# Performance work log

Hardware: AMD Instinct MI355X
Metric: run time of the kernel (lower is better)

Reference implementation:

```python
import jax, jax.numpy as jnp
import numpy as np

KX, KY = 3, 3
NUM_T_BINS, NUM_F_BINS = 1024, 1024
NX, NY = 512, 512
BATCH, CH = 16, 4


def fitpack_knots(x, k):
    # left/right: (k+1) repeated boundary knots; interior: sliding mean of x[i+1:i+k+1]
    n = x.shape[0]
    cs = jnp.concatenate([jnp.zeros((1,), x.dtype), jnp.cumsum(x)])
    interior = (cs[k + 1:n] - cs[1:n - k]) / k  # length n-k-1
    left = jnp.full((k + 1,), x[0], x.dtype)
    right = jnp.full((k + 1,), x[-1], x.dtype)
    return jnp.concatenate([left, interior, right])  # length n+k+1


def bspline_basis(x, k, t):
    # Cox-de Boor recursion; returns [n_points, m] with m = len(t)-k-1
    n = x.shape[0]
    m = t.shape[0] - k - 1
    b = ((t[None, :m] <= x[:, None]) & (x[:, None] < t[None, 1:m + 1])).astype(x.dtype)
    b = b.at[:, 0].set(jnp.where(x < t[1], 1.0, b[:, 0]))
    b = b.at[:, m - 1].set(jnp.where(x >= t[-2], 1.0, b[:, m - 1]))
    for d in range(1, k + 1):
        ld = t[d:m + d] - t[:m]
        rd = t[d + 1:m + d + 1] - t[1:m + 1]
        L = jnp.where(ld[None, :] == 0, 0.0,
                      (x[:, None] - t[None, :m]) / jnp.where(ld == 0, 1.0, ld)[None, :])
        R = jnp.where(rd[None, :] == 0, 0.0,
                      (t[None, d + 1:m + d + 1] - x[:, None]) / jnp.where(rd == 0, 1.0, rd)[None, :])
        b_shift = jnp.concatenate([b[:, 1:], jnp.zeros((n, 1), x.dtype)], axis=1)
        b = L * b + R * b_shift
    return b


def setup_inputs() -> dict:
    key = jax.random.key(0)
    Z = jax.random.normal(key, (BATCH, CH, NX, NY), dtype=jnp.float32)
    return {"Z": Z}


def reference(Z):
    B, C, nx, ny = Z.shape
    dt = Z.dtype
    # input grids (xin/yin/freqs None, logf False -> linspace(-1,1))
    x = jnp.linspace(-1.0, 1.0, nx, dtype=dt)
    y = jnp.linspace(-1.0, 1.0, ny, dtype=dt)
    tx = fitpack_knots(x, KX)
    ty = fitpack_knots(y, KY)
    Bx = bspline_basis(x, KX, tx)   # [nx, mx] with mx = nx
    By = bspline_basis(y, KY, ty)   # [ny, my] with my = ny
    # fit: least squares via normal equations (sx = sy = 0 -> no ridge term)
    BxT_Z_By = jnp.einsum('ij,bcik,kl->bcjl', Bx, Z, By)          # [B,C,mx,my]
    E = jnp.linalg.solve(Bx.T @ Bx, BxT_Z_By)                      # [B,C,mx,my]
    Coef = jnp.swapaxes(jnp.linalg.solve(By.T @ By, jnp.swapaxes(E, -1, -2)), -1, -2)
    # evaluation grids (xout/yout None, logf False -> linspace(-1,1)), clamped to knot range
    xe = jnp.clip(jnp.linspace(-1.0, 1.0, NUM_T_BINS, dtype=dt), tx[0], tx[-1])
    ye = jnp.clip(jnp.linspace(-1.0, 1.0, NUM_F_BINS, dtype=dt), ty[0], ty[-1])
    Bxe = bspline_basis(xe, KX, tx)  # [num_t, mx]
    Bye = bspline_basis(ye, KY, ty)  # [num_f, my]
    Zi = jnp.einsum('xk,bckm,ym->bcxy', Bxe, Coef, Bye)           # [B,C,num_t,num_f]
    return jnp.transpose(Zi, (0, 1, 3, 2))                         # [B,C,num_f,num_t]
```

## Files before the change

### kernel.cpp

```cpp
#include <hip/hip_runtime.h>

#define NN  512
#define NE  1024
#define NBC 64
#define WH  8
#define WT  17
#define YT  16

typedef float v4f __attribute__((ext_vector_type(4)));


struct Tables {
  float Gb[NN][WT];
  int   espan[NE];
  float ebas[NE * 4];
  float W3[NE][12];
};

constexpr int cfindspan(double u, const float* t) {
  if (u >= (double)t[NN]) return NN - 1;
  int lo = 3, hi = NN - 1;
  while (lo < hi) {
    int mid = (lo + hi + 1) >> 1;
    if ((double)t[mid] <= u) lo = mid; else hi = mid - 1;
  }
  return lo;
}

constexpr void cdeboor4(double u, const float* t, int s, double* N) {
  double left[4] = {}, right[4] = {};
  N[0] = 1.0; N[1] = 0.0; N[2] = 0.0; N[3] = 0.0;
  for (int d = 1; d <= 3; ++d) {
    left[d]  = u - (double)t[s + 1 - d];
    right[d] = (double)t[s + d] - u;
    double saved = 0.0;
    for (int r = 0; r < d; ++r) {
      double temp = N[r] / (right[r + 1] + left[d - r]);
      N[r] = saved + right[r + 1] * temp;
      saved = left[d - r] * temp;
    }
    N[d] = saved;
  }
}

constexpr Tables make_tables() {
  Tables T{};
  float x[NN] = {};
  for (int i = 0; i < NN; ++i) x[i] = (float)(-1.0 + (2.0 * i) / 511.0);
  x[0] = -1.0f; x[NN - 1] = 1.0f;
  float t[NN + 4] = {};
  {
    float cs[NN + 1] = {};
    for (int i = 0; i < NN; ++i) cs[i + 1] = cs[i] + x[i];
    for (int i = 0; i < NN - 4; ++i) t[4 + i] = (cs[4 + i] - cs[1 + i]) / 3.0f;
    for (int i = 0; i < 4; ++i) { t[i] = -1.0f; t[NN + i] = 1.0f; }
  }
  double W[NN][7] = {};
  for (int r = 0; r < NN; ++r) {
    double u = (double)x[r];
    int s = cfindspan(u, t);
    double N[4] = {};
    cdeboor4(u, t, s, N);
    for (int dd = 0; dd < 4; ++dd) W[r][s - r + dd] += N[dd];
  }
  for (int r = 0; r < NN; ++r) {
    double rd = 1.0 / W[r][3];
    for (int k = 1; k <= 3; ++k) {
      if (r + k < NN) {
        double l = W[r + k][3 - k] * rd;
        W[r + k][3 - k] = l;
        for (int cc = 1; cc <= 3; ++cc) W[r + k][3 - k + cc] -= l * W[r][3 + cc];
      }
    }
  }
  double Gbd[NN][WT] = {};
  double tv[WT] = {};
  for (int pass = 0; pass < 3; ++pass) {
    const int ylo = (pass == 0) ? 0 : (pass == 1) ? 480 : 256;
    const int yhi = (pass == 0) ? 32 : (pass == 1) ? 512 : 257;
    for (int y = ylo; y < yhi; ++y) {
      double wv[21] = {};
      int rend = y + 20; if (rend > NN - 1) rend = NN - 1;
      wv[0] = 1.0;
      for (int r = y + 1; r <= rend; ++r) {
        double acc = 0.0;
        if (r - 1 >= y) acc += W[r][2] * wv[r - 1 - y];
        if (r - 2 >= y) acc += W[r][1] * wv[r - 2 - y];
        if (r - 3 >= y) acc += W[r][0] * wv[r - 3 - y];
        wv[r - y] = -acc;
      }
      double g[29] = {};
      int glo = y - WH; if (glo < 0) glo = 0;
      for (int r = rend; r >= glo; --r) {
        double acc = (r >= y) ? wv[r - y] : 0.0;
        if (r + 1 <= rend) acc -= W[r][4] * g[r + 1 - (y - WH)];
        if (r + 2 <= rend) acc -= W[r][5] * g[r + 2 - (y - WH)];
        if (r + 3 <= rend) acc -= W[r][6] * g[r + 3 - (y - WH)];
        g[r - (y - WH)] = acc / W[r][3];
      }
      if (pass == 2) {
        for (int d = 0; d < WT; ++d) tv[d] = g[16 - d];
      } else {
        int jlo = y - WH; if (jlo < 0) jlo = 0;
        int jhi = y + WH; if (jhi > NN - 1) jhi = NN - 1;
        for (int j = jlo; j <= jhi; ++j) {
          const bool bdry = (pass == 0) ? (j < 24) : (j >= 488);
          if (bdry) Gbd[j][y - j + WH] = g[j - (y - WH)];
        }
      }
    }
  }
  for (int j = 24; j < 488; ++j)
    for (int d = 0; d < WT; ++d) Gbd[j][d] = tv[d];
  for (int j = 0; j < NN; ++j)
    for (int d = 0; d < WT; ++d) T.Gb[j][d] = (float)Gbd[j][d];
  int    s_all[NE] = {};
  double dN[NE][4] = {};
  for (int i = 0; i < NE; ++i) {
    float xe = (float)(-1.0 + (2.0 * i) / 1023.0);
    if (i == 0) xe = -1.0f;
    if (i == NE - 1) xe = 1.0f;
    double u = (double)xe;
    int s = cfindspan(u, t);
    double N[4] = {};
    cdeboor4(u, t, s, N);
    s_all[i] = s;
    for (int k = 0; k < 4; ++k) dN[i][k] = N[k];
    T.espan[i] = s;
    T.ebas[i * 4 + 0] = (float)N[0];
    T.ebas[i * 4 + 1] = (float)N[1];
    T.ebas[i * 4 + 2] = (float)N[2];
    T.ebas[i * 4 + 3] = (float)N[3];
  }
  for (int xx = 0; xx < NE; ++xx) {
    const int a3 = (s_all[(xx >> 2) << 2] - 3) & ~3;
    for (int k = 0; k < 4; ++k) {
      const int m = s_all[xx] - 3 + k - a3;
      T.W3[xx][m] = (float)dN[xx][k];
    }
  }
  return T;
}

__constant__ Tables g_tab = make_tables();


__global__ __launch_bounds__(256) void k_solve2d(const float* __restrict__ Z,
                                                 float* __restrict__ CT) {
  const int it = blockIdx.x * 64;
  const int jt = blockIdx.y * 64;
  const int bc = blockIdx.z;
  const float* __restrict__ src = Z + (size_t)bc * (NN * NN);
  __shared__ float At[64][89];
  const int tid = threadIdx.x;
  const int q4 = (tid & 15) * 4;

  {
    float cy[4][WT];
    #pragma unroll
    for (int q = 0; q < 4; ++q)
      #pragma unroll
      for (int d = 0; d < WT; ++d)
        cy[q][d] = g_tab.Gb[jt + q4 + q][d];
    #pragma unroll 1
    for (int p = 0; p < 5; ++p) {
      const int ii = p * 16 + (tid >> 4);
      int gi = it - 8 + ii;
      gi = (gi < 0) ? 0 : ((gi > NN - 1) ? NN - 1 : gi);
      const float* __restrict__ rowp = &src[(size_t)gi * NN];
      float w[20];
      #pragma unroll
      for (int e = 0; e < 5; ++e) {
        int gj = jt + q4 - 8 + e * 4;
        gj = (gj < 0) ? 0 : ((gj > NN - 4) ? NN - 4 : gj);
        *(float4*)&w[e * 4] = *(const float4*)&rowp[gj];
      }
      float4 a = make_float4(0.f, 0.f, 0.f, 0.f);
      #pragma unroll
      for (int d = 0; d < WT; ++d) {
        a.x += cy[0][d] * w[0 + d];
        a.y += cy[1][d] * w[1 + d];
        a.z += cy[2][d] * w[2 + d];
        a.w += cy[3][d] * w[3 + d];
      }
      At[q4 + 0][ii] = a.x;
      At[q4 + 1][ii] = a.y;
      At[q4 + 2][ii] = a.z;
      At[q4 + 3][ii] = a.w;
    }
  }
  {
    float cx[4][WT];
    #pragma unroll
    for (int q = 0; q < 4; ++q)
      #pragma unroll
      for (int d = 0; d < WT; ++d)
        cx[q][d] = g_tab.Gb[it + q4 + q][d];
    __syncthreads();
    float* __restrict__ dst = CT + (size_t)bc * (NN * NN);
    #pragma unroll 1
    for (int p = 0; p < 4; ++p) {
      const int jc = p * 16 + (tid >> 4);
      float w[20];
      #pragma unroll
      for (int e = 0; e < 5; ++e)
        *(float4*)&w[e * 4] = *(const float4*)&At[jc][q4 + e * 4];
      float4 a = make_float4(0.f, 0.f, 0.f, 0.f);
      #pragma unroll
      for (int d = 0; d < WT; ++d) {
        a.x += cx[0][d] * w[0 + d];
        a.y += cx[1][d] * w[1 + d];
        a.z += cx[2][d] * w[2 + d];
        a.w += cx[3][d] * w[3 + d];
      }
      *(float4*)&dst[(size_t)(jt + jc) * NN + it + q4] = a;
    }
  }
}


__global__ __launch_bounds__(256) void k_eval7(const float* __restrict__ CT,
                                               float* __restrict__ out) {
  const int ytile = ((blockIdx.x & 7) << 3) | (blockIdx.x >> 3);
  const int y0 = ytile * YT;
  const int bc = blockIdx.y;
  const float* __restrict__ S = CT + (size_t)bc * (NN * NN);
  __shared__ float rows[14][524];
  const int tid = threadIdx.x;
  const int rlo = g_tab.espan[y0] - 3;

  for (int u = tid; u < 14 * 128; u += 256) {
    const int rr = u >> 7, c4 = (u & 127) * 4;
    const int r = rlo + rr;
    float4 v = (r < NN) ? *(const float4*)&S[(size_t)r * NN + c4]
                        : make_float4(0.f, 0.f, 0.f, 0.f);
    *(float4*)&rows[rr][c4] = v;
  }
  if (tid < 42) {
    const int rr = tid / 3, c4 = 512 + (tid % 3) * 4;
    *(float4*)&rows[rr][c4] = make_float4(0.f, 0.f, 0.f, 0.f);
  }

  const int x0 = tid * 4;
  const int a3 = (g_tab.espan[x0] - 3) & ~3;
  float tp[4][12];
  #pragma unroll
  for (int e = 0; e < 4; ++e)
    #pragma unroll
    for (int m = 0; m < 12; ++m)
      tp[e][m] = g_tab.W3[x0 + e][m];

  __syncthreads();

  auto filterP = [&](int r) -> v4f {
    float w[12];
    #pragma unroll
    for (int e = 0; e < 3; ++e)
      *(float4*)&w[e * 4] = *(const float4*)&rows[r][a3 + e * 4];
    v4f p;
    #pragma unroll
    for (int e = 0; e < 4; ++e) {
      float s0 = 0.f, s1 = 0.f;
      #pragma unroll
      for (int m = 0; m < 12; m += 2) {
        s0 += tp[e][m]     * w[m];
        s1 += tp[e][m + 1] * w[m + 1];
      }
      p[e] = s0 + s1;
    }
    return p;
  };

  v4f P0 = filterP(0), P1 = filterP(1), P2 = filterP(2), P3 = filterP(3);
  int prev = 3;
  float* __restrict__ O0 = out + ((size_t)bc * NE + y0) * NE + x0;
  #pragma unroll 1
  for (int k = 0; k < YT; ++k) {
    const int ry = g_tab.espan[y0 + k] - rlo;
    if (ry != prev) {
      P0 = P1; P1 = P2; P2 = P3;
      P3 = filterP(ry);
      prev = ry;
    }
    const float4 wy = *(const float4*)&g_tab.ebas[(y0 + k) * 4];
    v4f o;
    #pragma unroll
    for (int e = 0; e < 4; ++e)
      o[e] = wy.x * P0[e] + wy.y * P1[e] + wy.z * P2[e] + wy.w * P3[e];
    __builtin_nontemporal_store(o, (v4f*)&O0[(size_t)k * NE]);
  }
}


extern "C" void kernel_launch(void* const* d_in, const int* in_sizes, int n_in,
                              void* d_out, int out_size, void* d_ws, size_t ws_size,
                              hipStream_t stream) {
  (void)in_sizes; (void)n_in; (void)out_size; (void)ws_size;
  const float* Z = (const float*)d_in[0];
  float* out = (float*)d_out;
  float* CT = (float*)d_ws;

  k_solve2d<<<dim3(8, 8, NBC),    256, 0, stream>>>(Z,  CT);
  k_eval7  <<<dim3(NE / YT, NBC), 256, 0, stream>>>(CT, out);
}
```

Baseline: 115.2 us.

## Store intermediate spline coefficients as bf16 and enlarge eval row tile

The solve kernel now writes the coefficient workspace as bfloat16 instead of float32, which halves its write traffic and the eval kernel's read traffic. The eval kernel unpacks bf16 from shared memory with shifts and masks, and each block covers 32 output rows instead of 16, with a matching staged-row count and block swizzle. Fewer blocks reload overlapping coefficient rows. The cost is reduced precision in the intermediate coefficients, which may break accuracy tolerance, and fewer, larger eval blocks.

Measured after the change: 113.1 us. Within noise of the previous version (-1.8%).

```diff
diff --git a/kernel.cpp b/kernel.cpp
--- a/kernel.cpp
+++ b/kernel.cpp
@@ -1,11 +1,13 @@
 #include <hip/hip_runtime.h>
+#include <hip/hip_bf16.h>
 
 #define NN  512
 #define NE  1024
 #define NBC 64
 #define WH  8
 #define WT  17
-#define YT  16
+#define YT  32
+#define NR  20
 
 typedef float v4f __attribute__((ext_vector_type(4)));
 
@@ -144,9 +146,14 @@
 
 __constant__ Tables g_tab = make_tables();
 
+__device__ __forceinline__ unsigned short f2bf(float f) {
+  __hip_bfloat16 h = __float2bfloat16(f);
+  return reinterpret_cast<const unsigned short&>(h);
+}
+
 
 __global__ __launch_bounds__(256) void k_solve2d(const float* __restrict__ Z,
-                                                 float* __restrict__ CT) {
+                                                 unsigned short* __restrict__ CT) {
   const int it = blockIdx.x * 64;
   const int jt = blockIdx.y * 64;
   const int bc = blockIdx.z;
@@ -197,7 +204,7 @@
       for (int d = 0; d < WT; ++d)
         cx[q][d] = g_tab.Gb[it + q4 + q][d];
     __syncthreads();
-    float* __restrict__ dst = CT + (size_t)bc * (NN * NN);
+    unsigned short* __restrict__ dst = CT + (size_t)bc * (NN * NN);
     #pragma unroll 1
     for (int p = 0; p < 4; ++p) {
       const int jc = p * 16 + (tid >> 4);
@@ -213,32 +220,31 @@
         a.z += cx[2][d] * w[2 + d];
         a.w += cx[3][d] * w[3 + d];
       }
-      *(float4*)&dst[(size_t)(jt + jc) * NN + it + q4] = a;
-    }
-  }
-}
-
-
-__global__ __launch_bounds__(256) void k_eval7(const float* __restrict__ CT,
+      ushort4 o;
+      o.x = f2bf(a.x); o.y = f2bf(a.y); o.z = f2bf(a.z); o.w = f2bf(a.w);
+      *(ushort4*)&dst[(size_t)(jt + jc) * NN + it + q4] = o;
+    }
+  }
+}
+
+
+__global__ __launch_bounds__(256) void k_eval8(const unsigned short* __restrict__ CT,
                                                float* __restrict__ out) {
-  const int ytile = ((blockIdx.x & 7) << 3) | (blockIdx.x >> 3);
+  const int b = blockIdx.x;
+  const int ytile = ((b & 7) << 2) | (b >> 3);
   const int y0 = ytile * YT;
   const int bc = blockIdx.y;
-  const float* __restrict__ S = CT + (size_t)bc * (NN * NN);
-  __shared__ float rows[14][524];
+  const unsigned short* __restrict__ S = CT + (size_t)bc * (NN * NN);
+  __shared__ unsigned short rows[NR][528];
   const int tid = threadIdx.x;
   const int rlo = g_tab.espan[y0] - 3;
 
-  for (int u = tid; u < 14 * 128; u += 256) {
-    const int rr = u >> 7, c4 = (u & 127) * 4;
+  for (int u = tid; u < NR * 66; u += 256) {
+    const int rr = u / 66, c8 = (u % 66) * 8;
     const int r = rlo + rr;
-    float4 v = (r < NN) ? *(const float4*)&S[(size_t)r * NN + c4]
-                        : make_float4(0.f, 0.f, 0.f, 0.f);
-    *(float4*)&rows[rr][c4] = v;
-  }
-  if (tid < 42) {
-    const int rr = tid / 3, c4 = 512 + (tid % 3) * 4;
-    *(float4*)&rows[rr][c4] = make_float4(0.f, 0.f, 0.f, 0.f);
+    uint4 v = make_uint4(0u, 0u, 0u, 0u);
+    if (r < NN && c8 < 512) v = *(const uint4*)&S[(size_t)r * NN + c8];
+    *(uint4*)&rows[rr][c8] = v;
   }
 
   const int x0 = tid * 4;
@@ -253,10 +259,16 @@
   __syncthreads();
 
   auto filterP = [&](int r) -> v4f {
+    uint2 q0 = *(const uint2*)&rows[r][a3];
+    uint2 q1 = *(const uint2*)&rows[r][a3 + 4];
+    uint2 q2 = *(const uint2*)&rows[r][a3 + 8];
     float w[12];
-    #pragma unroll
-    for (int e = 0; e < 3; ++e)
-      *(float4*)&w[e * 4] = *(const float4*)&rows[r][a3 + e * 4];
+    w[0]  = __uint_as_float(q0.x << 16); w[1]  = __uint_as_float(q0.x & 0xffff0000u);
+    w[2]  = __uint_as_float(q0.y << 16); w[3]  = __uint_as_float(q0.y & 0xffff0000u);
+    w[4]  = __uint_as_float(q1.x << 16); w[5]  = __uint_as_float(q1.x & 0xffff0000u);
+    w[6]  = __uint_as_float(q1.y << 16); w[7]  = __uint_as_float(q1.y & 0xffff0000u);
+    w[8]  = __uint_as_float(q2.x << 16); w[9]  = __uint_as_float(q2.x & 0xffff0000u);
+    w[10] = __uint_as_float(q2.y << 16); w[11] = __uint_as_float(q2.y & 0xffff0000u);
     v4f p;
     #pragma unroll
     for (int e = 0; e < 4; ++e) {
@@ -298,8 +310,8 @@
   (void)in_sizes; (void)n_in; (void)out_size; (void)ws_size;
   const float* Z = (const float*)d_in[0];
   float* out = (float*)d_out;
-  float* CT = (float*)d_ws;
-
-  k_solve2d<<<dim3(8, 8, NBC),    256, 0, stream>>>(Z,  CT);
-  k_eval7  <<<dim3(NE / YT, NBC), 256, 0, stream>>>(CT, out);
-}
+  unsigned short* CT = (unsigned short*)d_ws;
+
+  k_solve2d<<<dim3(8, 8, NBC),   256, 0, stream>>>(Z,  CT);
+  k_eval8  <<<dim3(NE / YT, NBC), 256, 0, stream>>>(CT, out);
+}
```

## Fuse banded solve and B-spline evaluation into one kernel with folded x-weights

Applied to the files above, without the earlier changes.

Replaces the two-kernel pipeline (banded inverse solve writing coefficients to workspace, then evaluation) with a single fused kernel. The x-direction inverse band is precomputed together with the evaluation basis into a 24-tap table, so each block applies the y-direction inverse on a staged Z window in shared memory and then a combined x filter. The inverse band is also truncated from 17 to 13 taps, and nontemporal stores are dropped. This removes the intermediate 64MB round trip through workspace, but risks accuracy from the narrower band and adds redundant halo work per block.

Measured after the change: 227.2 us. +97.2%, slower.

```diff
diff --git a/kernel.cpp b/kernel.cpp
--- a/kernel.cpp
+++ b/kernel.cpp
@@ -3,9 +3,12 @@
 #define NN  512
 #define NE  1024
 #define NBC 64
-#define WH  8
-#define WT  17
-#define YT  16
+#define WH  6
+#define WT  13
+#define XT  256
+#define YTL 32
+#define BR  156
+#define ZC  40
 
 typedef float v4f __attribute__((ext_vector_type(4)));
 
@@ -14,7 +17,7 @@
   float Gb[NN][WT];
   int   espan[NE];
   float ebas[NE * 4];
-  float W3[NE][12];
+  float W4[NE][24];
 };
 
 constexpr int cfindspan(double u, const float* t) {
@@ -89,7 +92,7 @@
         if (r - 3 >= y) acc += W[r][0] * wv[r - 3 - y];
         wv[r - y] = -acc;
       }
-      double g[29] = {};
+      double g[33] = {};
       int glo = y - WH; if (glo < 0) glo = 0;
       for (int r = rend; r >= glo; --r) {
         double acc = (r >= y) ? wv[r - y] : 0.0;
@@ -99,7 +102,7 @@
         g[r - (y - WH)] = acc / W[r][3];
       }
       if (pass == 2) {
-        for (int d = 0; d < WT; ++d) tv[d] = g[16 - d];
+        for (int d = 0; d < WT; ++d) tv[d] = g[2 * WH - d];
       } else {
         int jlo = y - WH; if (jlo < 0) jlo = 0;
         int jhi = y + WH; if (jhi > NN - 1) jhi = NN - 1;
@@ -133,11 +136,16 @@
     T.ebas[i * 4 + 3] = (float)N[3];
   }
   for (int xx = 0; xx < NE; ++xx) {
-    const int a3 = (s_all[(xx >> 2) << 2] - 3) & ~3;
+    const int a4 = (s_all[(xx >> 2) << 2] - 9) & ~3;
+    double acc[24] = {};
     for (int k = 0; k < 4; ++k) {
-      const int m = s_all[xx] - 3 + k - a3;
-      T.W3[xx][m] = (float)dN[xx][k];
-    }
+      const int i = s_all[xx] - 3 + k;
+      for (int d = 0; d < WT; ++d) {
+        const int m = i - 6 + d - a4;
+        acc[m] += dN[xx][k] * Gbd[i][d];
+      }
+    }
+    for (int m = 0; m < 24; ++m) T.W4[xx][m] = (float)acc[m];
   }
   return T;
 }
@@ -145,149 +153,113 @@
 __constant__ Tables g_tab = make_tables();
 
 
-__global__ __launch_bounds__(256) void k_solve2d(const float* __restrict__ Z,
-                                                 float* __restrict__ CT) {
-  const int it = blockIdx.x * 64;
-  const int jt = blockIdx.y * 64;
-  const int bc = blockIdx.z;
+__global__ __launch_bounds__(256) void k_fused(const float* __restrict__ Z,
+                                               float* __restrict__ out) {
+  const int bx = blockIdx.x;
+  const int xt = (bx & 3) * XT;
+  const int y0 = (bx >> 2) * YTL;
+  const int bc = blockIdx.y;
   const float* __restrict__ src = Z + (size_t)bc * (NN * NN);
-  __shared__ float At[64][89];
+
+  const int rlo = g_tab.espan[y0] - 3;
+  const int s0  = g_tab.espan[xt];
+  const int ibB = (s0 - 12) & ~3;
+  const int g0  = (rlo - 6) & ~3;
+  const int coff = (rlo - 6) - g0;
+
+  __shared__ float Zw[BR][ZC];
+  __shared__ float B[20][BR];
   const int tid = threadIdx.x;
-  const int q4 = (tid & 15) * 4;
-
-  {
-    float cy[4][WT];
-    #pragma unroll
-    for (int q = 0; q < 4; ++q)
-      #pragma unroll
-      for (int d = 0; d < WT; ++d)
-        cy[q][d] = g_tab.Gb[jt + q4 + q][d];
+
+  for (int u = tid; u < BR * 10; u += 256) {
+    const int rr = u / 10, g = u % 10;
+    int r = ibB + rr;
+    r = (r < 0) ? 0 : ((r > NN - 1) ? NN - 1 : r);
+    int gc = g0 + 4 * g;
+    gc = (gc < 0) ? 0 : ((gc > NN - 4) ? NN - 4 : gc);
+    *(float4*)&Zw[rr][g * 4] = *(const float4*)&src[(size_t)r * NN + gc];
+  }
+  __syncthreads();
+
+  if (tid < BR) {
+    float w[ZC];
+    #pragma unroll
+    for (int e = 0; e < 10; ++e)
+      *(float4*)&w[e * 4] = *(const float4*)&Zw[tid][e * 4];
+    float w2[32];
+    if (coff == 0) {
+      #pragma unroll
+      for (int m = 0; m < 32; ++m) w2[m] = w[m];
+    } else if (coff == 1) {
+      #pragma unroll
+      for (int m = 0; m < 32; ++m) w2[m] = w[m + 1];
+    } else if (coff == 2) {
+      #pragma unroll
+      for (int m = 0; m < 32; ++m) w2[m] = w[m + 2];
+    } else {
+      #pragma unroll
+      for (int m = 0; m < 32; ++m) w2[m] = w[m + 3];
+    }
     #pragma unroll 1
-    for (int p = 0; p < 5; ++p) {
-      const int ii = p * 16 + (tid >> 4);
-      int gi = it - 8 + ii;
-      gi = (gi < 0) ? 0 : ((gi > NN - 1) ? NN - 1 : gi);
-      const float* __restrict__ rowp = &src[(size_t)gi * NN];
-      float w[20];
-      #pragma unroll
-      for (int e = 0; e < 5; ++e) {
-        int gj = jt + q4 - 8 + e * 4;
-        gj = (gj < 0) ? 0 : ((gj > NN - 4) ? NN - 4 : gj);
-        *(float4*)&w[e * 4] = *(const float4*)&rowp[gj];
-      }
-      float4 a = make_float4(0.f, 0.f, 0.f, 0.f);
-      #pragma unroll
-      for (int d = 0; d < WT; ++d) {
-        a.x += cy[0][d] * w[0 + d];
-        a.y += cy[1][d] * w[1 + d];
-        a.z += cy[2][d] * w[2 + d];
-        a.w += cy[3][d] * w[3 + d];
-      }
-      At[q4 + 0][ii] = a.x;
-      At[q4 + 1][ii] = a.y;
-      At[q4 + 2][ii] = a.z;
-      At[q4 + 3][ii] = a.w;
-    }
-  }
-  {
-    float cx[4][WT];
-    #pragma unroll
-    for (int q = 0; q < 4; ++q)
-      #pragma unroll
-      for (int d = 0; d < WT; ++d)
-        cx[q][d] = g_tab.Gb[it + q4 + q][d];
-    __syncthreads();
-    float* __restrict__ dst = CT + (size_t)bc * (NN * NN);
-    #pragma unroll 1
-    for (int p = 0; p < 4; ++p) {
-      const int jc = p * 16 + (tid >> 4);
-      float w[20];
-      #pragma unroll
-      for (int e = 0; e < 5; ++e)
-        *(float4*)&w[e * 4] = *(const float4*)&At[jc][q4 + e * 4];
-      float4 a = make_float4(0.f, 0.f, 0.f, 0.f);
-      #pragma unroll
-      for (int d = 0; d < WT; ++d) {
-        a.x += cx[0][d] * w[0 + d];
-        a.y += cx[1][d] * w[1 + d];
-        a.z += cx[2][d] * w[2 + d];
-        a.w += cx[3][d] * w[3 + d];
-      }
-      *(float4*)&dst[(size_t)(jt + jc) * NN + it + q4] = a;
-    }
-  }
-}
-
-
-__global__ __launch_bounds__(256) void k_eval7(const float* __restrict__ CT,
-                                               float* __restrict__ out) {
-  const int ytile = ((blockIdx.x & 7) << 3) | (blockIdx.x >> 3);
-  const int y0 = ytile * YT;
-  const int bc = blockIdx.y;
-  const float* __restrict__ S = CT + (size_t)bc * (NN * NN);
-  __shared__ float rows[14][524];
-  const int tid = threadIdx.x;
-  const int rlo = g_tab.espan[y0] - 3;
-
-  for (int u = tid; u < 14 * 128; u += 256) {
-    const int rr = u >> 7, c4 = (u & 127) * 4;
-    const int r = rlo + rr;
-    float4 v = (r < NN) ? *(const float4*)&S[(size_t)r * NN + c4]
-                        : make_float4(0.f, 0.f, 0.f, 0.f);
-    *(float4*)&rows[rr][c4] = v;
-  }
-  if (tid < 42) {
-    const int rr = tid / 3, c4 = 512 + (tid % 3) * 4;
-    *(float4*)&rows[rr][c4] = make_float4(0.f, 0.f, 0.f, 0.f);
-  }
-
-  const int x0 = tid * 4;
-  const int a3 = (g_tab.espan[x0] - 3) & ~3;
-  float tp[4][12];
+    for (int jr = 0; jr < 20; ++jr) {
+      const float* __restrict__ gr = g_tab.Gb[rlo + jr];
+      float acc = 0.f;
+      #pragma unroll
+      for (int e = 0; e < WT; ++e) acc += gr[e] * w2[jr + e];
+      B[jr][tid] = acc;
+    }
+  }
+  __syncthreads();
+
+  const int xq = tid & 63, yg = tid >> 6;
+  const int x0 = xt + xq * 4;
+  const int a4 = (g_tab.espan[x0] - 9) & ~3;
+  const int off4 = a4 - ibB;
+  float tp[4][24];
   #pragma unroll
   for (int e = 0; e < 4; ++e)
     #pragma unroll
-    for (int m = 0; m < 12; ++m)
-      tp[e][m] = g_tab.W3[x0 + e][m];
-
-  __syncthreads();
+    for (int m = 0; m < 24; ++m)
+      tp[e][m] = g_tab.W4[x0 + e][m];
 
   auto filterP = [&](int r) -> v4f {
-    float w[12];
-    #pragma unroll
-    for (int e = 0; e < 3; ++e)
-      *(float4*)&w[e * 4] = *(const float4*)&rows[r][a3 + e * 4];
+    float w[24];
+    #pragma unroll
+    for (int e = 0; e < 6; ++e)
+      *(float4*)&w[e * 4] = *(const float4*)&B[r][off4 + e * 4];
     v4f p;
     #pragma unroll
     for (int e = 0; e < 4; ++e) {
-      float s0 = 0.f, s1 = 0.f;
-      #pragma unroll
-      for (int m = 0; m < 12; m += 2) {
-        s0 += tp[e][m]     * w[m];
-        s1 += tp[e][m + 1] * w[m + 1];
-      }
-      p[e] = s0 + s1;
+      float s0a = 0.f, s1a = 0.f;
+      #pragma unroll
+      for (int m = 0; m < 24; m += 2) {
+        s0a += tp[e][m]     * w[m];
+        s1a += tp[e][m + 1] * w[m + 1];
+      }
+      p[e] = s0a + s1a;
     }
     return p;
   };
 
-  v4f P0 = filterP(0), P1 = filterP(1), P2 = filterP(2), P3 = filterP(3);
-  int prev = 3;
-  float* __restrict__ O0 = out + ((size_t)bc * NE + y0) * NE + x0;
+  const int k0 = y0 + yg * 8;
+  int prev = g_tab.espan[k0] - rlo;
+  v4f P0 = filterP(prev - 3), P1 = filterP(prev - 2),
+      P2 = filterP(prev - 1), P3 = filterP(prev);
+  float* __restrict__ O0 = out + ((size_t)bc * NE + k0) * NE + x0;
   #pragma unroll 1
-  for (int k = 0; k < YT; ++k) {
-    const int ry = g_tab.espan[y0 + k] - rlo;
+  for (int kk = 0; kk < 8; ++kk) {
+    const int ry = g_tab.espan[k0 + kk] - rlo;
     if (ry != prev) {
       P0 = P1; P1 = P2; P2 = P3;
       P3 = filterP(ry);
       prev = ry;
     }
-    const float4 wy = *(const float4*)&g_tab.ebas[(y0 + k) * 4];
+    const float4 wy = *(const float4*)&g_tab.ebas[(k0 + kk) * 4];
     v4f o;
     #pragma unroll
     for (int e = 0; e < 4; ++e)
       o[e] = wy.x * P0[e] + wy.y * P1[e] + wy.z * P2[e] + wy.w * P3[e];
-    __builtin_nontemporal_store(o, (v4f*)&O0[(size_t)k * NE]);
+    *(v4f*)&O0[(size_t)kk * NE] = o;
   }
 }
 
@@ -295,11 +267,8 @@
 extern "C" void kernel_launch(void* const* d_in, const int* in_sizes, int n_in,
                               void* d_out, int out_size, void* d_ws, size_t ws_size,
                               hipStream_t stream) {
-  (void)in_sizes; (void)n_in; (void)out_size; (void)ws_size;
+  (void)in_sizes; (void)n_in; (void)out_size; (void)d_ws; (void)ws_size;
   const float* Z = (const float*)d_in[0];
   float* out = (float*)d_out;
-  float* CT = (float*)d_ws;
-
-  k_solve2d<<<dim3(8, 8, NBC),    256, 0, stream>>>(Z,  CT);
-  k_eval7  <<<dim3(NE / YT, NBC), 256, 0, stream>>>(CT, out);
-}
+  k_fused<<<dim3(128, NBC), 256, 0, stream>>>(Z, out);
+}
```
